# Kernel tuning notes

Hardware: AMD Instinct MI355X
Metric: run time of the kernel (lower is better)

The kernel has to match this reference:

```python
import jax, jax.numpy as jnp
import numpy as np

B, P, Q, D = 16, 4096, 1024, 256


def setup_inputs() -> dict:
    key = jax.random.key(0)
    k1, k2, k3, k4 = jax.random.split(key, 4)
    return {
        "passage_encodes": jax.random.normal(k1, (B, P, D), dtype=jnp.float32),
        "question_encodes": jax.random.normal(k2, (B, Q, D), dtype=jnp.float32),
        "w_attn": jax.random.normal(k3, (2 * D, 1), dtype=jnp.float32) * (1.0 / np.sqrt(2 * D)),
        "b_attn": jnp.zeros((1,), dtype=jnp.float32),
        "w_out": jax.random.normal(k4, (2 * D, 256), dtype=jnp.float32) * (1.0 / np.sqrt(2 * D)),
        "b_out": jnp.zeros((256,), dtype=jnp.float32),
    }


def reference(passage_encodes, question_encodes, w_attn, b_attn, w_out, b_out):
    # similarity matrix [B, P, Q]
    sim = jnp.einsum('bpd,bqd->bpq', passage_encodes, question_encodes)
    # context-to-question attention
    c2q = jax.nn.softmax(sim, axis=-1)                       # [B, P, Q]
    ctx2q = jnp.einsum('bpq,bqd->bpd', c2q, question_encodes)  # [B, P, D]
    # question-to-context attention (softmax over row-max)
    q2c = jax.nn.softmax(jnp.max(sim, axis=-1), axis=-1)     # [B, P]
    q2c_vec = jnp.einsum('bp,bpd->bd', q2c, passage_encodes)  # [B, D]
    tp = jnp.tanh(passage_encodes)
    concat = jnp.concatenate([
        tp * jnp.tanh(ctx2q),
        tp * jnp.tanh(q2c_vec)[:, None, :],  # broadcast instead of repeat
    ], axis=-1)                                              # [B, P, 2D]
    # attention reducer: linear -> softmax over sequence -> weighted sum
    w = jax.nn.softmax(jnp.einsum('bpc,co->bp', concat, w_attn) + b_attn[0], axis=1)
    reduced = jnp.einsum('bp,bpc->bc', w, concat)            # [B, 2D]
    return reduced @ w_out + b_out                            # [B, output_dim]
```

## Files before the change

kernel.cpp:

```cpp
#include <hip/hip_runtime.h>
#include <cmath>

#define BB 16
#define PP 4096
#define QQ 1024
#define DD 256

typedef __attribute__((ext_vector_type(8))) short short8;
typedef __attribute__((ext_vector_type(4))) float floatx4;
typedef __attribute__((ext_vector_type(4))) _Float16 half4;

static __device__ inline ushort bf16_rne(float x) {
  unsigned u = __float_as_uint(x);
  unsigned r = (u + 0x7fffu + ((u >> 16) & 1u)) >> 16;
  return (ushort)r;
}
static __device__ inline float bf16f(ushort h) { return __uint_as_float(((unsigned)h) << 16); }

static __device__ inline float ftanh(float x) {
  float e = __expf(2.0f * x);
  return 1.0f - 2.0f * __builtin_amdgcn_rcpf(e + 1.0f);
}

static __device__ inline void gl16(const void* g, void* l) {
  __builtin_amdgcn_global_load_lds(
      (const __attribute__((address_space(1))) unsigned int*)g,
      (__attribute__((address_space(3))) unsigned int*)l, 16, 0, 0);
}

__global__ __launch_bounds__(256) void kQprep(
    const float* __restrict__ ques, ushort* __restrict__ qb)
{
  const int b = blockIdx.y, qt = blockIdx.x;
  __shared__ float tile[32][260];
  const int tid = threadIdx.x;
  const float* src = ques + ((size_t)b * QQ + qt * 32) * DD;
  for (int i = tid; i < 32 * 64; i += 256) {
    int r = i >> 6, c = (i & 63) << 2;
    *(float4*)&tile[r][c] = *(const float4*)(src + r * DD + c);
  }
  __syncthreads();
  ushort* blob = qb + (size_t)(b * 32 + qt) * 24576;
  {
    int r = tid >> 3;
    int j0 = (tid & 7) * 4;
#pragma unroll
    for (int jj = 0; jj < 4; ++jj) {
      int j = j0 + jj;
      ushort h8[8], l8[8];
#pragma unroll
      for (int e = 0; e < 8; ++e) {
        float x = tile[r][j * 8 + e];
        ushort h = bf16_rne(x);
        h8[e] = h; l8[e] = bf16_rne(x - bf16f(h));
      }
      int g = r * 32 + (j ^ (r & 7));
      *(uint4*)&blob[(size_t)g * 8] = *(uint4*)h8;
      *(uint4*)&blob[8192 + (size_t)g * 8] = *(uint4*)l8;
    }
  }
  {
    int d = tid;
    int s = (d >> 1) & 3;
    ushort h32[32];
#pragma unroll
    for (int r = 0; r < 32; ++r) h32[r] = bf16_rne(tile[r][d]);
#pragma unroll
    for (int k = 0; k < 4; ++k)
      *(uint4*)&blob[16384 + (size_t)d * 32 + (k ^ s) * 8] = *(uint4*)&h32[k * 8];
  }
}

__global__ __launch_bounds__(512, 1) void kA(
    const float* __restrict__ pass, const ushort* __restrict__ qb,
    const float* __restrict__ w_attn,
    _Float16* __restrict__ first_h, _Float16* __restrict__ tp_h,
    float* __restrict__ rowmax, float* __restrict__ logit1)
{
  __shared__ alignas(16) char sm[147456];

  const int b    = blockIdx.y;
  const int p0   = blockIdx.x * 128;
  const int tid  = threadIdx.x;
  const int w    = tid >> 6;
  const int lane = tid & 63;
  const int l15  = lane & 15;
  const int quad = lane >> 4;
  const int swz  = l15 & 7;

  short8 bhi[8], blo[8];
  {
    const float* prow = pass + (((size_t)b * PP + p0 + w * 16 + l15) * DD);
#pragma unroll
    for (int c = 0; c < 8; ++c) {
      const float* p8 = prow + c * 32 + quad * 8;
      float4 x0 = *(const float4*)p8;
      float4 x1 = *(const float4*)(p8 + 4);
      float xs[8] = {x0.x, x0.y, x0.z, x0.w, x1.x, x1.y, x1.z, x1.w};
#pragma unroll
      for (int j = 0; j < 8; ++j) {
        ushort h = bf16_rne(xs[j]);
        ushort lo = bf16_rne(xs[j] - bf16f(h));
        bhi[c][j] = (short)h;
        blo[c][j] = (short)lo;
      }
    }
  }

  int goff[8];
#pragma unroll
  for (int c = 0; c < 8; ++c) goff[c] = (l15 * 32 + ((4 * c + quad) ^ swz)) * 8;
  const int vtoff = l15 * 32 + ((quad ^ ((l15 >> 1) & 3)) * 8);

  const ushort* tb = qb + (size_t)b * 32 * 24576;
  const int dma_l = w * 3072 + lane * 8;
  const int dma_s = w * 6144 + lane * 16;

  floatx4 accO[16];
#pragma unroll
  for (int i = 0; i < 16; ++i) accO[i] = (floatx4){0.f, 0.f, 0.f, 0.f};
  float mx = -INFINITY, ps = 0.f;
  short8 phi = {0, 0, 0, 0, 0, 0, 0, 0}, plo = {0, 0, 0, 0, 0, 0, 0, 0};

  {
    const ushort* gs = tb + dma_l;
    char* ld = sm + dma_s;
#pragma unroll
    for (int i = 0; i < 6; ++i) gl16(gs + i * 512, ld + i * 1024);
  }
  __syncthreads();

  for (int t = 0; t < 32; ++t) {
    const int ic = t % 3, ip = (t + 2) % 3, inx = (t + 1) % 3;
    char* cur = sm + ic * 49152;
    char* prv = sm + ip * 49152;
    if (t < 31) {
      const ushort* gs = tb + (size_t)(t + 1) * 24576 + dma_l;
      char* ld = sm + inx * 49152 + dma_s;
#pragma unroll
      for (int i = 0; i < 6; ++i) gl16(gs + i * 512, ld + i * 1024);
    }

    const ushort* Qhi = (const ushort*)cur;
    const ushort* Qlo = (const ushort*)(cur + 16384);
    floatx4 s0 = (floatx4){0.f, 0.f, 0.f, 0.f};
    floatx4 s1 = (floatx4){0.f, 0.f, 0.f, 0.f};
#pragma unroll
    for (int c = 0; c < 8; ++c) {
      short8 a0h = *(const short8*)&Qhi[goff[c]];
      short8 a0l = *(const short8*)&Qlo[goff[c]];
      short8 a1h = *(const short8*)&Qhi[goff[c] + 4096];
      short8 a1l = *(const short8*)&Qlo[goff[c] + 4096];
      s0 = __builtin_amdgcn_mfma_f32_16x16x32_bf16(a0h, bhi[c], s0, 0, 0, 0);
      s0 = __builtin_amdgcn_mfma_f32_16x16x32_bf16(a0h, blo[c], s0, 0, 0, 0);
      s0 = __builtin_amdgcn_mfma_f32_16x16x32_bf16(a0l, bhi[c], s0, 0, 0, 0);
      s1 = __builtin_amdgcn_mfma_f32_16x16x32_bf16(a1h, bhi[c], s1, 0, 0, 0);
      s1 = __builtin_amdgcn_mfma_f32_16x16x32_bf16(a1h, blo[c], s1, 0, 0, 0);
      s1 = __builtin_amdgcn_mfma_f32_16x16x32_bf16(a1l, bhi[c], s1, 0, 0, 0);
    }

    if (t > 0) {
      const ushort* TQ = (const ushort*)(prv + 32768);
#pragma unroll
      for (int nt = 0; nt < 16; ++nt) {
        short8 vhi = *(const short8*)&TQ[nt * 512 + vtoff];
        accO[nt] = __builtin_amdgcn_mfma_f32_16x16x32_bf16(phi, vhi, accO[nt], 0, 0, 0);
        accO[nt] = __builtin_amdgcn_mfma_f32_16x16x32_bf16(plo, vhi, accO[nt], 0, 0, 0);
      }
    }

    float pv[8];
#pragma unroll
    for (int r = 0; r < 4; ++r) {
      float s = s0[r];
      mx = fmaxf(mx, s);
      pv[r] = __expf(s - 60.f);
      ps += pv[r];
    }
#pragma unroll
    for (int r = 0; r < 4; ++r) {
      float s = s1[r];
      mx = fmaxf(mx, s);
      pv[4 + r] = __expf(s - 60.f);
      ps += pv[4 + r];
    }

    unsigned* pwv = (unsigned*)prv + w * 512;
#pragma unroll
    for (int mt = 0; mt < 2; ++mt) {
      unsigned pk[4];
#pragma unroll
      for (int r = 0; r < 4; ++r) {
        float x = pv[mt * 4 + r];
        ushort h = bf16_rne(x);
        ushort lo = bf16_rne(x - bf16f(h));
        pk[r] = (unsigned)h | ((unsigned)lo << 16);
      }
      int g = l15 * 8 + ((mt * 4 + quad) ^ swz);
      *(uint4*)&pwv[g * 4] = *(uint4*)pk;
    }
    uint4 u0 = *(const uint4*)&pwv[(l15 * 8 + ((2 * quad) ^ swz)) * 4];
    uint4 u1 = *(const uint4*)&pwv[(l15 * 8 + ((2 * quad + 1) ^ swz)) * 4];
    unsigned ua[8] = {u0.x, u0.y, u0.z, u0.w, u1.x, u1.y, u1.z, u1.w};
#pragma unroll
    for (int j = 0; j < 8; ++j) {
      phi[j] = (short)(ua[j] & 0xffffu);
      plo[j] = (short)(ua[j] >> 16);
    }
    __syncthreads();
  }

  {
    const ushort* TQ = (const ushort*)(sm + 49152 + 32768);
#pragma unroll
    for (int nt = 0; nt < 16; ++nt) {
      short8 vhi = *(const short8*)&TQ[nt * 512 + vtoff];
      accO[nt] = __builtin_amdgcn_mfma_f32_16x16x32_bf16(phi, vhi, accO[nt], 0, 0, 0);
      accO[nt] = __builtin_amdgcn_mfma_f32_16x16x32_bf16(plo, vhi, accO[nt], 0, 0, 0);
    }
  }

  ps += __shfl_xor(ps, 16);
  ps += __shfl_xor(ps, 32);
  mx = fmaxf(mx, __shfl_xor(mx, 16));
  mx = fmaxf(mx, __shfl_xor(mx, 32));

  __syncthreads();
  float* Of = (float*)(sm + w * 16640);
#pragma unroll
  for (int nt = 0; nt < 16; ++nt)
#pragma unroll
    for (int r = 0; r < 4; ++r)
      Of[(quad * 4 + r) * 260 + nt * 16 + l15] = accO[nt][r];
  const float4 w1 = *(const float4*)(w_attn + lane * 4);
  const size_t rowoff = (size_t)b * PP + p0 + w * 16;
#pragma unroll
  for (int j = 0; j < 16; ++j) {
    float4 o = *(const float4*)&Of[j * 260 + lane * 4];
    float linv = 1.f / __shfl(ps, j);
    float4 pv4 = *(const float4*)(pass + (rowoff + j) * DD + lane * 4);
    float tpx = ftanh(pv4.x), tpy = ftanh(pv4.y), tpz = ftanh(pv4.z), tpw = ftanh(pv4.w);
    float4 f;
    f.x = tpx * ftanh(o.x * linv);
    f.y = tpy * ftanh(o.y * linv);
    f.z = tpz * ftanh(o.z * linv);
    f.w = tpw * ftanh(o.w * linv);
    half4 fh = {(_Float16)f.x, (_Float16)f.y, (_Float16)f.z, (_Float16)f.w};
    half4 th = {(_Float16)tpx, (_Float16)tpy, (_Float16)tpz, (_Float16)tpw};
    *(half4*)(first_h + (rowoff + j) * DD + lane * 4) = fh;
    *(half4*)(tp_h + (rowoff + j) * DD + lane * 4) = th;
    float part = f.x * w1.x + f.y * w1.y + f.z * w1.z + f.w * w1.w;
    part += __shfl_xor(part, 1);  part += __shfl_xor(part, 2);
    part += __shfl_xor(part, 4);  part += __shfl_xor(part, 8);
    part += __shfl_xor(part, 16); part += __shfl_xor(part, 32);
    if (lane == 0) logit1[rowoff + j] = part;
  }
  if (lane < 16) rowmax[rowoff + lane] = mx;
}

__global__ __launch_bounds__(256) void kB2(
    const float* __restrict__ pass, const float* __restrict__ rowmax,
    float* __restrict__ numpart, float* __restrict__ denpart)
{
  const int b = blockIdx.y, chunk = blockIdx.x;
  const int tid = threadIdx.x, r = tid >> 6, ln = tid & 63;
  __shared__ float sacc[4][64][4];
  __shared__ float sden[4][64];
  const float* rm = rowmax + (size_t)b * PP + chunk * 128;
  const float* pb = pass + ((size_t)b * PP + chunk * 128) * DD;
  float4 acc = make_float4(0.f, 0.f, 0.f, 0.f);
  float den = 0.f;
  for (int p = r; p < 128; p += 4) {
    float wgt = __expf(rm[p] - 60.f);
    float4 v = *(const float4*)(pb + (size_t)p * DD + ln * 4);
    acc.x += wgt * v.x; acc.y += wgt * v.y;
    acc.z += wgt * v.z; acc.w += wgt * v.w;
    den += wgt;
  }
  *(float4*)&sacc[r][ln][0] = acc;
  sden[r][ln] = den;
  __syncthreads();
  if (r == 0) {
    float4 s;
    s.x = sacc[0][ln][0] + sacc[1][ln][0] + sacc[2][ln][0] + sacc[3][ln][0];
    s.y = sacc[0][ln][1] + sacc[1][ln][1] + sacc[2][ln][1] + sacc[3][ln][1];
    s.z = sacc[0][ln][2] + sacc[1][ln][2] + sacc[2][ln][2] + sacc[3][ln][2];
    s.w = sacc[0][ln][3] + sacc[1][ln][3] + sacc[2][ln][3] + sacc[3][ln][3];
    *(float4*)(numpart + (size_t)(chunk * 16 + b) * DD + ln * 4) = s;
    if (ln == 0)
      denpart[chunk * 16 + b] = sden[0][0] + sden[1][0] + sden[2][0] + sden[3][0];
  }
}

__global__ void kB3(const float* __restrict__ numpart, const float* __restrict__ denpart,
                    const float* __restrict__ w_attn,
                    float* __restrict__ tq, float* __restrict__ w2tq)
{
  const int b = blockIdx.x, d = threadIdx.x;
  float den = 0.f, num = 0.f;
#pragma unroll
  for (int c = 0; c < 32; ++c) {
    den += denpart[c * 16 + b];
    num += numpart[(size_t)(c * 16 + b) * DD + d];
  }
  float t = ftanh(num / den);
  tq[b * DD + d] = t;
  w2tq[b * DD + d] = w_attn[DD + d] * t;
}

__global__ __launch_bounds__(256) void kC(
    const _Float16* __restrict__ tp_h, const float* __restrict__ logit1,
    const float* __restrict__ w2tq, float* __restrict__ el)
{
  const int b = blockIdx.y, chunk = blockIdx.x;
  const int wave = threadIdx.x >> 6, lane = threadIdx.x & 63;
  const float4 wv = *(const float4*)(w2tq + b * DD + (lane << 2));
  const int pbase = chunk * 128 + wave * 32;
  for (int j = 0; j < 32; ++j) {
    int p = pbase + j;
    half4 tv = *(const half4*)(tp_h + ((size_t)b * PP + p) * DD + (lane << 2));
    float part = (float)tv.x * wv.x + (float)tv.y * wv.y +
                 (float)tv.z * wv.z + (float)tv.w * wv.w;
    part += __shfl_xor(part, 1);  part += __shfl_xor(part, 2);
    part += __shfl_xor(part, 4);  part += __shfl_xor(part, 8);
    part += __shfl_xor(part, 16); part += __shfl_xor(part, 32);
    if (lane == 0)
      el[(size_t)b * PP + p] = __expf(logit1[(size_t)b * PP + p] + part);
  }
}

__global__ __launch_bounds__(256) void kE(
    const _Float16* __restrict__ tp_h, const _Float16* __restrict__ first_h,
    const float* __restrict__ el,
    float* __restrict__ r1part, float* __restrict__ r2part, float* __restrict__ den2part)
{
  const int b = blockIdx.y, chunk = blockIdx.x;
  const int tid = threadIdx.x, r = tid >> 6, ln = tid & 63;
  __shared__ float s1[4][64][4];
  __shared__ float s2[4][64][4];
  __shared__ float sd[4][64];
  const float* ev = el + (size_t)b * PP + chunk * 128;
  const size_t base = ((size_t)b * PP + chunk * 128) * DD;
  float a1[4] = {0.f, 0.f, 0.f, 0.f}, a2[4] = {0.f, 0.f, 0.f, 0.f};
  float den = 0.f;
  for (int p = r; p < 128; p += 4) {
    float wgt = ev[p];
    half4 f = *(const half4*)(first_h + base + (size_t)p * DD + ln * 4);
    half4 t = *(const half4*)(tp_h + base + (size_t)p * DD + ln * 4);
    a1[0] += wgt * (float)f.x; a1[1] += wgt * (float)f.y;
    a1[2] += wgt * (float)f.z; a1[3] += wgt * (float)f.w;
    a2[0] += wgt * (float)t.x; a2[1] += wgt * (float)t.y;
    a2[2] += wgt * (float)t.z; a2[3] += wgt * (float)t.w;
    den += wgt;
  }
  *(float4*)&s1[r][ln][0] = *(float4*)a1;
  *(float4*)&s2[r][ln][0] = *(float4*)a2;
  sd[r][ln] = den;
  __syncthreads();
  if (r == 0) {
    float o1[4], o2[4];
#pragma unroll
    for (int i = 0; i < 4; ++i) {
      o1[i] = s1[0][ln][i] + s1[1][ln][i] + s1[2][ln][i] + s1[3][ln][i];
      o2[i] = s2[0][ln][i] + s2[1][ln][i] + s2[2][ln][i] + s2[3][ln][i];
    }
    *(float4*)(r1part + (size_t)(chunk * 16 + b) * DD + ln * 4) = *(float4*)o1;
    *(float4*)(r2part + (size_t)(chunk * 16 + b) * DD + ln * 4) = *(float4*)o2;
    if (ln == 0)
      den2part[chunk * 16 + b] = sd[0][0] + sd[1][0] + sd[2][0] + sd[3][0];
  }
}

__global__ __launch_bounds__(256) void kF(
    const float* __restrict__ r1part, const float* __restrict__ r2part,
    const float* __restrict__ den2part, const float* __restrict__ tq,
    const float* __restrict__ w_out, const float* __restrict__ b_out,
    float* __restrict__ out)
{
  const int b = blockIdx.x, o = threadIdx.x;
  __shared__ float R1[256], R2[256];
  float den = 0.f, red1 = 0.f, red2 = 0.f;
#pragma unroll
  for (int c = 0; c < 32; ++c) {
    den += den2part[c * 16 + b];
    red1 += r1part[(size_t)(c * 16 + b) * DD + o];
    red2 += r2part[(size_t)(c * 16 + b) * DD + o];
  }
  float inv = 1.f / den;
  R1[o] = red1 * inv;
  R2[o] = red2 * inv * tq[b * DD + o];
  __syncthreads();
  float acc = b_out[o];
  for (int k = 0; k < DD; ++k)
    acc += R1[k] * w_out[k * 256 + o];
  for (int k = 0; k < DD; ++k)
    acc += R2[k] * w_out[(DD + k) * 256 + o];
  out[b * 256 + o] = acc;
}

extern "C" void kernel_launch(void* const* d_in, const int* in_sizes, int n_in,
                              void* d_out, int out_size, void* d_ws, size_t ws_size,
                              hipStream_t stream) {
  const float* pass   = (const float*)d_in[0];
  const float* ques   = (const float*)d_in[1];
  const float* w_attn = (const float*)d_in[2];
  const float* w_out  = (const float*)d_in[4];
  const float* b_out  = (const float*)d_in[5];
  float* out = (float*)d_out;

  float* ws       = (float*)d_ws;
  float* rowmax   = ws;
  float* logit1   = rowmax   + (size_t)BB * PP;
  float* el       = logit1   + (size_t)BB * PP;
  float* numpart  = el       + (size_t)BB * PP;
  float* denpart  = numpart  + (size_t)32 * BB * DD;
  float* r1part   = denpart  + 32 * BB;
  float* r2part   = r1part   + (size_t)32 * BB * DD;
  float* den2part = r2part   + (size_t)32 * BB * DD;
  float* tq       = den2part + 32 * BB;
  float* w2tq     = tq       + BB * DD;
  ushort* qbb     = (ushort*)(w2tq + BB * DD);
  _Float16* first_h = (_Float16*)(qbb + (size_t)BB * 32 * 24576);
  _Float16* tp_h    = first_h + (size_t)BB * PP * DD;

  kQprep<<<dim3(QQ / 32, BB), 256, 0, stream>>>(ques, qbb);
  kA    <<<dim3(PP / 128, BB), 512, 0, stream>>>(pass, qbb, w_attn,
                                                 first_h, tp_h, rowmax, logit1);
  kB2   <<<dim3(32, BB), 256, 0, stream>>>(pass, rowmax, numpart, denpart);
  kB3   <<<BB, 256, 0, stream>>>(numpart, denpart, w_attn, tq, w2tq);
  kC    <<<dim3(32, BB), 256, 0, stream>>>(tp_h, logit1, w2tq, el);
  kE    <<<dim3(32, BB), 256, 0, stream>>>(tp_h, first_h, el, r1part, r2part, den2part);
  kF    <<<BB, 256, 0, stream>>>(r1part, r2part, den2part, tq, w_out, b_out, out);
}
```

Baseline: 352.3 us.

## Re-tile attention kernel warps over Q halves and D groups with LDS P exchange

Each warp now computes scores for two 16-row passage tiles against one half of each Q chunk, so Q fragments are reused across two tiles. P is written to a shared LDS buffer and the PV product is split so each warp accumulates a 64x64 output block. Partial sums and maxes are combined through LDS. The triple buffer becomes a double buffer, shared memory shrinks, launch bounds request two blocks per CU, and setprio hints are added. The cost is an extra barrier per iteration, and the PV step now runs in the same iteration as the scores instead of being overlapped one step behind.

After: 381.1 us. 8.2% more time.

```diff
diff --git a/kernel.cpp b/kernel.cpp
--- a/kernel.cpp
+++ b/kernel.cpp
@@ -9,6 +9,7 @@
 typedef __attribute__((ext_vector_type(8))) short short8;
 typedef __attribute__((ext_vector_type(4))) float floatx4;
 typedef __attribute__((ext_vector_type(4))) _Float16 half4;
+typedef __attribute__((ext_vector_type(4))) unsigned short ushort4v;
 
 static __device__ inline ushort bf16_rne(float x) {
   unsigned u = __float_as_uint(x);
@@ -71,13 +72,13 @@
   }
 }
 
-__global__ __launch_bounds__(512, 1) void kA(
+__global__ __launch_bounds__(512, 2) void kA(
     const float* __restrict__ pass, const ushort* __restrict__ qb,
     const float* __restrict__ w_attn,
     _Float16* __restrict__ first_h, _Float16* __restrict__ tp_h,
     float* __restrict__ rowmax, float* __restrict__ logit1)
 {
-  __shared__ alignas(16) char sm[147456];
+  __shared__ alignas(16) char sm[135168];
 
   const int b    = blockIdx.y;
   const int p0   = blockIdx.x * 128;
@@ -88,9 +89,15 @@
   const int quad = lane >> 4;
   const int swz  = l15 & 7;
 
-  short8 bhi[8], blo[8];
-  {
-    const float* prow = pass + (((size_t)b * PP + p0 + w * 16 + l15) * DD);
+  const int qt1  = w >> 2;
+  const int pt1  = (w & 3) * 2;
+  const int dgrp = w >> 1;
+  const int phs  = (w & 1) * 4;
+
+  short8 bhi[2][8], blo[2][8];
+#pragma unroll
+  for (int pt = 0; pt < 2; ++pt) {
+    const float* prow = pass + (((size_t)b * PP + p0 + (pt1 + pt) * 16 + l15) * DD);
 #pragma unroll
     for (int c = 0; c < 8; ++c) {
       const float* p8 = prow + c * 32 + quad * 8;
@@ -99,28 +106,32 @@
       float xs[8] = {x0.x, x0.y, x0.z, x0.w, x1.x, x1.y, x1.z, x1.w};
 #pragma unroll
       for (int j = 0; j < 8; ++j) {
-        ushort h = bf16_rne(xs[j]);
+        ushort h  = bf16_rne(xs[j]);
         ushort lo = bf16_rne(xs[j] - bf16f(h));
-        bhi[c][j] = (short)h;
-        blo[c][j] = (short)lo;
+        bhi[pt][c][j] = (short)h;
+        blo[pt][c][j] = (short)lo;
       }
     }
   }
 
-  int goff[8];
-#pragma unroll
-  for (int c = 0; c < 8; ++c) goff[c] = (l15 * 32 + ((4 * c + quad) ^ swz)) * 8;
+  const int gb    = (qt1 * 16 + l15) * 256;
   const int vtoff = l15 * 32 + ((quad ^ ((l15 >> 1) & 3)) * 8);
+
+  ushort* PbufH = (ushort*)(sm + 98304);
+  ushort* PbufL = (ushort*)(sm + 106496);
+  const int pgd  = qt1 * 2 + (quad >> 1);
+  const int psub = (quad & 1) * 4;
 
   const ushort* tb = qb + (size_t)b * 32 * 24576;
   const int dma_l = w * 3072 + lane * 8;
   const int dma_s = w * 6144 + lane * 16;
 
-  floatx4 accO[16];
-#pragma unroll
-  for (int i = 0; i < 16; ++i) accO[i] = (floatx4){0.f, 0.f, 0.f, 0.f};
-  float mx = -INFINITY, ps = 0.f;
-  short8 phi = {0, 0, 0, 0, 0, 0, 0, 0}, plo = {0, 0, 0, 0, 0, 0, 0, 0};
+  floatx4 accO[4][4];
+#pragma unroll
+  for (int i = 0; i < 4; ++i)
+#pragma unroll
+    for (int k = 0; k < 4; ++k) accO[i][k] = (floatx4){0.f, 0.f, 0.f, 0.f};
+  float ps0 = 0.f, ps1 = 0.f, mx0 = -INFINITY, mx1 = -INFINITY;
 
   {
     const ushort* gs = tb + dma_l;
@@ -131,12 +142,10 @@
   __syncthreads();
 
   for (int t = 0; t < 32; ++t) {
-    const int ic = t % 3, ip = (t + 2) % 3, inx = (t + 1) % 3;
-    char* cur = sm + ic * 49152;
-    char* prv = sm + ip * 49152;
+    const char* cur = sm + (t & 1) * 49152;
     if (t < 31) {
       const ushort* gs = tb + (size_t)(t + 1) * 24576 + dma_l;
-      char* ld = sm + inx * 49152 + dma_s;
+      char* ld = sm + ((t + 1) & 1) * 49152 + dma_s;
 #pragma unroll
       for (int i = 0; i < 6; ++i) gl16(gs + i * 512, ld + i * 1024);
     }
@@ -145,99 +154,114 @@
     const ushort* Qlo = (const ushort*)(cur + 16384);
     floatx4 s0 = (floatx4){0.f, 0.f, 0.f, 0.f};
     floatx4 s1 = (floatx4){0.f, 0.f, 0.f, 0.f};
+    __builtin_amdgcn_s_setprio(1);
 #pragma unroll
     for (int c = 0; c < 8; ++c) {
-      short8 a0h = *(const short8*)&Qhi[goff[c]];
-      short8 a0l = *(const short8*)&Qlo[goff[c]];
-      short8 a1h = *(const short8*)&Qhi[goff[c] + 4096];
-      short8 a1l = *(const short8*)&Qlo[goff[c] + 4096];
-      s0 = __builtin_amdgcn_mfma_f32_16x16x32_bf16(a0h, bhi[c], s0, 0, 0, 0);
-      s0 = __builtin_amdgcn_mfma_f32_16x16x32_bf16(a0h, blo[c], s0, 0, 0, 0);
-      s0 = __builtin_amdgcn_mfma_f32_16x16x32_bf16(a0l, bhi[c], s0, 0, 0, 0);
-      s1 = __builtin_amdgcn_mfma_f32_16x16x32_bf16(a1h, bhi[c], s1, 0, 0, 0);
-      s1 = __builtin_amdgcn_mfma_f32_16x16x32_bf16(a1h, blo[c], s1, 0, 0, 0);
-      s1 = __builtin_amdgcn_mfma_f32_16x16x32_bf16(a1l, bhi[c], s1, 0, 0, 0);
-    }
-
-    if (t > 0) {
-      const ushort* TQ = (const ushort*)(prv + 32768);
-#pragma unroll
-      for (int nt = 0; nt < 16; ++nt) {
-        short8 vhi = *(const short8*)&TQ[nt * 512 + vtoff];
-        accO[nt] = __builtin_amdgcn_mfma_f32_16x16x32_bf16(phi, vhi, accO[nt], 0, 0, 0);
-        accO[nt] = __builtin_amdgcn_mfma_f32_16x16x32_bf16(plo, vhi, accO[nt], 0, 0, 0);
+      const int go = gb + (((4 * c + quad) ^ swz) << 3);
+      short8 ah = *(const short8*)&Qhi[go];
+      short8 al = *(const short8*)&Qlo[go];
+      s0 = __builtin_amdgcn_mfma_f32_16x16x32_bf16(ah, bhi[0][c], s0, 0, 0, 0);
+      s0 = __builtin_amdgcn_mfma_f32_16x16x32_bf16(ah, blo[0][c], s0, 0, 0, 0);
+      s0 = __builtin_amdgcn_mfma_f32_16x16x32_bf16(al, bhi[0][c], s0, 0, 0, 0);
+      s1 = __builtin_amdgcn_mfma_f32_16x16x32_bf16(ah, bhi[1][c], s1, 0, 0, 0);
+      s1 = __builtin_amdgcn_mfma_f32_16x16x32_bf16(ah, blo[1][c], s1, 0, 0, 0);
+      s1 = __builtin_amdgcn_mfma_f32_16x16x32_bf16(al, bhi[1][c], s1, 0, 0, 0);
+    }
+    __builtin_amdgcn_s_setprio(0);
+
+    {
+      ushort4v ph, pl;
+#pragma unroll
+      for (int r = 0; r < 4; ++r) {
+        float s = s0[r];
+        mx0 = fmaxf(mx0, s);
+        float x = __expf(s - 60.f);
+        ps0 += x;
+        ushort h = bf16_rne(x);
+        ph[r] = h;
+        pl[r] = bf16_rne(x - bf16f(h));
       }
-    }
-
-    float pv[8];
-#pragma unroll
-    for (int r = 0; r < 4; ++r) {
-      float s = s0[r];
-      mx = fmaxf(mx, s);
-      pv[r] = __expf(s - 60.f);
-      ps += pv[r];
-    }
-#pragma unroll
-    for (int r = 0; r < 4; ++r) {
-      float s = s1[r];
-      mx = fmaxf(mx, s);
-      pv[4 + r] = __expf(s - 60.f);
-      ps += pv[4 + r];
-    }
-
-    unsigned* pwv = (unsigned*)prv + w * 512;
-#pragma unroll
-    for (int mt = 0; mt < 2; ++mt) {
-      unsigned pk[4];
+      const int wi = ((pt1 * 16 + l15) * 4 + (pgd ^ (l15 & 3))) * 8 + psub;
+      *(ushort4v*)&PbufH[wi] = ph;
+      *(ushort4v*)&PbufL[wi] = pl;
+    }
+    {
+      ushort4v ph, pl;
 #pragma unroll
       for (int r = 0; r < 4; ++r) {
-        float x = pv[mt * 4 + r];
+        float s = s1[r];
+        mx1 = fmaxf(mx1, s);
+        float x = __expf(s - 60.f);
+        ps1 += x;
         ushort h = bf16_rne(x);
-        ushort lo = bf16_rne(x - bf16f(h));
-        pk[r] = (unsigned)h | ((unsigned)lo << 16);
+        ph[r] = h;
+        pl[r] = bf16_rne(x - bf16f(h));
       }
-      int g = l15 * 8 + ((mt * 4 + quad) ^ swz);
-      *(uint4*)&pwv[g * 4] = *(uint4*)pk;
-    }
-    uint4 u0 = *(const uint4*)&pwv[(l15 * 8 + ((2 * quad) ^ swz)) * 4];
-    uint4 u1 = *(const uint4*)&pwv[(l15 * 8 + ((2 * quad + 1) ^ swz)) * 4];
-    unsigned ua[8] = {u0.x, u0.y, u0.z, u0.w, u1.x, u1.y, u1.z, u1.w};
-#pragma unroll
-    for (int j = 0; j < 8; ++j) {
-      phi[j] = (short)(ua[j] & 0xffffu);
-      plo[j] = (short)(ua[j] >> 16);
-    }
+      const int wi = (((pt1 + 1) * 16 + l15) * 4 + (pgd ^ (l15 & 3))) * 8 + psub;
+      *(ushort4v*)&PbufH[wi] = ph;
+      *(ushort4v*)&PbufL[wi] = pl;
+    }
+
+    asm volatile("s_waitcnt lgkmcnt(0)" ::: "memory");
+    __builtin_amdgcn_s_barrier();
+    __builtin_amdgcn_sched_barrier(0);
+
+    const ushort* TQ = (const ushort*)(cur + 32768);
+    short8 vhi[4];
+#pragma unroll
+    for (int k = 0; k < 4; ++k)
+      vhi[k] = *(const short8*)&TQ[(dgrp * 4 + k) * 512 + vtoff];
+    __builtin_amdgcn_s_setprio(1);
+#pragma unroll
+    for (int pt = 0; pt < 4; ++pt) {
+      const int ri = (((phs + pt) * 16 + l15) * 4 + (quad ^ (l15 & 3))) * 8;
+      short8 phh = *(const short8*)&PbufH[ri];
+      short8 pll = *(const short8*)&PbufL[ri];
+#pragma unroll
+      for (int k = 0; k < 4; ++k) {
+        accO[pt][k] = __builtin_amdgcn_mfma_f32_16x16x32_bf16(phh, vhi[k], accO[pt][k], 0, 0, 0);
+        accO[pt][k] = __builtin_amdgcn_mfma_f32_16x16x32_bf16(pll, vhi[k], accO[pt][k], 0, 0, 0);
+      }
+    }
+    __builtin_amdgcn_s_setprio(0);
     __syncthreads();
   }
 
-  {
-    const ushort* TQ = (const ushort*)(sm + 49152 + 32768);
-#pragma unroll
-    for (int nt = 0; nt < 16; ++nt) {
-      short8 vhi = *(const short8*)&TQ[nt * 512 + vtoff];
-      accO[nt] = __builtin_amdgcn_mfma_f32_16x16x32_bf16(phi, vhi, accO[nt], 0, 0, 0);
-      accO[nt] = __builtin_amdgcn_mfma_f32_16x16x32_bf16(plo, vhi, accO[nt], 0, 0, 0);
-    }
-  }
-
-  ps += __shfl_xor(ps, 16);
-  ps += __shfl_xor(ps, 32);
-  mx = fmaxf(mx, __shfl_xor(mx, 16));
-  mx = fmaxf(mx, __shfl_xor(mx, 32));
-
-  __syncthreads();
-  float* Of = (float*)(sm + w * 16640);
-#pragma unroll
-  for (int nt = 0; nt < 16; ++nt)
-#pragma unroll
-    for (int r = 0; r < 4; ++r)
-      Of[(quad * 4 + r) * 260 + nt * 16 + l15] = accO[nt][r];
+  ps0 += __shfl_xor(ps0, 16); ps0 += __shfl_xor(ps0, 32);
+  ps1 += __shfl_xor(ps1, 16); ps1 += __shfl_xor(ps1, 32);
+  mx0 = fmaxf(mx0, __shfl_xor(mx0, 16)); mx0 = fmaxf(mx0, __shfl_xor(mx0, 32));
+  mx1 = fmaxf(mx1, __shfl_xor(mx1, 16)); mx1 = fmaxf(mx1, __shfl_xor(mx1, 32));
+
+  float* psb = (float*)(sm + 133120);
+  float* mxb = (float*)(sm + 134144);
+  if (lane < 16) {
+    psb[(qt1 * 8 + pt1) * 16 + l15]     = ps0;
+    psb[(qt1 * 8 + pt1 + 1) * 16 + l15] = ps1;
+    mxb[(qt1 * 8 + pt1) * 16 + l15]     = mx0;
+    mxb[(qt1 * 8 + pt1 + 1) * 16 + l15] = mx1;
+  }
+  __syncthreads();
+  const float pstot = psb[w * 16 + l15] + psb[128 + w * 16 + l15];
+  const float mxtot = fmaxf(mxb[w * 16 + l15], mxb[128 + w * 16 + l15]);
+  const size_t rowoff = (size_t)b * PP + p0 + w * 16;
+  if (lane < 16) rowmax[rowoff + lane] = mxtot;
+
+  float* Of = (float*)sm;
+#pragma unroll
+  for (int pt = 0; pt < 4; ++pt)
+#pragma unroll
+    for (int k = 0; k < 4; ++k)
+#pragma unroll
+      for (int r = 0; r < 4; ++r)
+        Of[((w & 1) * 64 + pt * 16 + quad * 4 + r) * 260 + dgrp * 64 + k * 16 + l15] =
+            accO[pt][k][r];
+  __syncthreads();
+
   const float4 w1 = *(const float4*)(w_attn + lane * 4);
-  const size_t rowoff = (size_t)b * PP + p0 + w * 16;
 #pragma unroll
   for (int j = 0; j < 16; ++j) {
-    float4 o = *(const float4*)&Of[j * 260 + lane * 4];
-    float linv = 1.f / __shfl(ps, j);
+    float4 o = *(const float4*)&Of[(w * 16 + j) * 260 + lane * 4];
+    float linv = 1.f / __shfl(pstot, j);
     float4 pv4 = *(const float4*)(pass + (rowoff + j) * DD + lane * 4);
     float tpx = ftanh(pv4.x), tpy = ftanh(pv4.y), tpz = ftanh(pv4.z), tpw = ftanh(pv4.w);
     float4 f;
@@ -255,7 +279,6 @@
     part += __shfl_xor(part, 16); part += __shfl_xor(part, 32);
     if (lane == 0) logit1[rowoff + j] = part;
   }
-  if (lane < 16) rowmax[rowoff + lane] = mx;
 }
 
 __global__ __launch_bounds__(256) void kB2(
```

## Fuse q2c reduction into attention kernel and logit exp into reducer

Applied to the files above, without the earlier changes.

The q2c weighted sum over passage rows moves into kA's epilogue. It reuses the passage row already loaded there and the row max held in registers, which removes kB2 and its second full read of the passage tensor. kC is folded into kE, which now computes the tp·w2tq dot product and the exp inline, so the separate el buffer and one extra read of tp_h go away. The hi part of the bf16 split is now made by truncation instead of round-to-nearest, so the lo residual compensates and precision stays the same. In exchange kA gets extra LDS reduction work and an extra barrier at its tail.

Result: faster. 328.3 us (-6.8%).

```diff
diff --git a/kernel.cpp b/kernel.cpp
--- a/kernel.cpp
+++ b/kernel.cpp
@@ -75,7 +75,8 @@
     const float* __restrict__ pass, const ushort* __restrict__ qb,
     const float* __restrict__ w_attn,
     _Float16* __restrict__ first_h, _Float16* __restrict__ tp_h,
-    float* __restrict__ rowmax, float* __restrict__ logit1)
+    float* __restrict__ logit1,
+    float* __restrict__ numpart, float* __restrict__ denpart)
 {
   __shared__ alignas(16) char sm[147456];
 
@@ -192,9 +193,10 @@
 #pragma unroll
       for (int r = 0; r < 4; ++r) {
         float x = pv[mt * 4 + r];
-        ushort h = bf16_rne(x);
-        ushort lo = bf16_rne(x - bf16f(h));
-        pk[r] = (unsigned)h | ((unsigned)lo << 16);
+        unsigned u = __float_as_uint(x);
+        unsigned hb = u & 0xffff0000u;
+        ushort lo = bf16_rne(x - __uint_as_float(hb));
+        pk[r] = (hb >> 16) | ((unsigned)lo << 16);
       }
       int g = l15 * 8 + ((mt * 4 + quad) ^ swz);
       *(uint4*)&pwv[g * 4] = *(uint4*)pk;
@@ -234,11 +236,17 @@
       Of[(quad * 4 + r) * 260 + nt * 16 + l15] = accO[nt][r];
   const float4 w1 = *(const float4*)(w_attn + lane * 4);
   const size_t rowoff = (size_t)b * PP + p0 + w * 16;
+  float4 qacc = make_float4(0.f, 0.f, 0.f, 0.f);
+  float dacc = 0.f;
 #pragma unroll
   for (int j = 0; j < 16; ++j) {
     float4 o = *(const float4*)&Of[j * 260 + lane * 4];
     float linv = 1.f / __shfl(ps, j);
     float4 pv4 = *(const float4*)(pass + (rowoff + j) * DD + lane * 4);
+    float wj = __expf(__shfl(mx, j) - 60.f);
+    qacc.x += wj * pv4.x; qacc.y += wj * pv4.y;
+    qacc.z += wj * pv4.z; qacc.w += wj * pv4.w;
+    dacc += wj;
     float tpx = ftanh(pv4.x), tpy = ftanh(pv4.y), tpz = ftanh(pv4.z), tpw = ftanh(pv4.w);
     float4 f;
     f.x = tpx * ftanh(o.x * linv);
@@ -255,40 +263,23 @@
     part += __shfl_xor(part, 16); part += __shfl_xor(part, 32);
     if (lane == 0) logit1[rowoff + j] = part;
   }
-  if (lane < 16) rowmax[rowoff + lane] = mx;
-}
-
-__global__ __launch_bounds__(256) void kB2(
-    const float* __restrict__ pass, const float* __restrict__ rowmax,
-    float* __restrict__ numpart, float* __restrict__ denpart)
-{
-  const int b = blockIdx.y, chunk = blockIdx.x;
-  const int tid = threadIdx.x, r = tid >> 6, ln = tid & 63;
-  __shared__ float sacc[4][64][4];
-  __shared__ float sden[4][64];
-  const float* rm = rowmax + (size_t)b * PP + chunk * 128;
-  const float* pb = pass + ((size_t)b * PP + chunk * 128) * DD;
-  float4 acc = make_float4(0.f, 0.f, 0.f, 0.f);
-  float den = 0.f;
-  for (int p = r; p < 128; p += 4) {
-    float wgt = __expf(rm[p] - 60.f);
-    float4 v = *(const float4*)(pb + (size_t)p * DD + ln * 4);
-    acc.x += wgt * v.x; acc.y += wgt * v.y;
-    acc.z += wgt * v.z; acc.w += wgt * v.w;
-    den += wgt;
-  }
-  *(float4*)&sacc[r][ln][0] = acc;
-  sden[r][ln] = den;
-  __syncthreads();
-  if (r == 0) {
-    float4 s;
-    s.x = sacc[0][ln][0] + sacc[1][ln][0] + sacc[2][ln][0] + sacc[3][ln][0];
-    s.y = sacc[0][ln][1] + sacc[1][ln][1] + sacc[2][ln][1] + sacc[3][ln][1];
-    s.z = sacc[0][ln][2] + sacc[1][ln][2] + sacc[2][ln][2] + sacc[3][ln][2];
-    s.w = sacc[0][ln][3] + sacc[1][ln][3] + sacc[2][ln][3] + sacc[3][ln][3];
-    *(float4*)(numpart + (size_t)(chunk * 16 + b) * DD + ln * 4) = s;
-    if (ln == 0)
-      denpart[chunk * 16 + b] = sden[0][0] + sden[1][0] + sden[2][0] + sden[3][0];
+
+  float* redw = (float*)(sm + w * 16640);
+  *(float4*)&redw[lane * 4] = qacc;
+  if (lane == 0) redw[256] = dacc;
+  __syncthreads();
+  if (w == 0) {
+    float4 s = make_float4(0.f, 0.f, 0.f, 0.f);
+    float dsum = 0.f;
+#pragma unroll
+    for (int wv = 0; wv < 8; ++wv) {
+      const float* rp = (const float*)(sm + wv * 16640);
+      float4 v = *(const float4*)&rp[lane * 4];
+      s.x += v.x; s.y += v.y; s.z += v.z; s.w += v.w;
+      dsum += rp[256];
+    }
+    *(float4*)(numpart + (size_t)(blockIdx.x * 16 + b) * DD + lane * 4) = s;
+    if (lane == 0) denpart[blockIdx.x * 16 + b] = dsum;
   }
 }
 
@@ -308,30 +299,9 @@
   w2tq[b * DD + d] = w_attn[DD + d] * t;
 }
 
-__global__ __launch_bounds__(256) void kC(
-    const _Float16* __restrict__ tp_h, const float* __restrict__ logit1,
-    const float* __restrict__ w2tq, float* __restrict__ el)
-{
-  const int b = blockIdx.y, chunk = blockIdx.x;
-  const int wave = threadIdx.x >> 6, lane = threadIdx.x & 63;
-  const float4 wv = *(const float4*)(w2tq + b * DD + (lane << 2));
-  const int pbase = chunk * 128 + wave * 32;
-  for (int j = 0; j < 32; ++j) {
-    int p = pbase + j;
-    half4 tv = *(const half4*)(tp_h + ((size_t)b * PP + p) * DD + (lane << 2));
-    float part = (float)tv.x * wv.x + (float)tv.y * wv.y +
-                 (float)tv.z * wv.z + (float)tv.w * wv.w;
-    part += __shfl_xor(part, 1);  part += __shfl_xor(part, 2);
-    part += __shfl_xor(part, 4);  part += __shfl_xor(part, 8);
-    part += __shfl_xor(part, 16); part += __shfl_xor(part, 32);
-    if (lane == 0)
-      el[(size_t)b * PP + p] = __expf(logit1[(size_t)b * PP + p] + part);
-  }
-}
-
 __global__ __launch_bounds__(256) void kE(
     const _Float16* __restrict__ tp_h, const _Float16* __restrict__ first_h,
-    const float* __restrict__ el,
+    const float* __restrict__ logit1, const float* __restrict__ w2tq,
     float* __restrict__ r1part, float* __restrict__ r2part, float* __restrict__ den2part)
 {
   const int b = blockIdx.y, chunk = blockIdx.x;
@@ -339,14 +309,20 @@
   __shared__ float s1[4][64][4];
   __shared__ float s2[4][64][4];
   __shared__ float sd[4][64];
-  const float* ev = el + (size_t)b * PP + chunk * 128;
+  const float4 wv = *(const float4*)(w2tq + b * DD + (ln << 2));
+  const float* lg = logit1 + (size_t)b * PP + chunk * 128;
   const size_t base = ((size_t)b * PP + chunk * 128) * DD;
   float a1[4] = {0.f, 0.f, 0.f, 0.f}, a2[4] = {0.f, 0.f, 0.f, 0.f};
   float den = 0.f;
   for (int p = r; p < 128; p += 4) {
-    float wgt = ev[p];
     half4 f = *(const half4*)(first_h + base + (size_t)p * DD + ln * 4);
     half4 t = *(const half4*)(tp_h + base + (size_t)p * DD + ln * 4);
+    float part = (float)t.x * wv.x + (float)t.y * wv.y +
+                 (float)t.z * wv.z + (float)t.w * wv.w;
+    part += __shfl_xor(part, 1);  part += __shfl_xor(part, 2);
+    part += __shfl_xor(part, 4);  part += __shfl_xor(part, 8);
+    part += __shfl_xor(part, 16); part += __shfl_xor(part, 32);
+    float wgt = __expf(lg[p] + part);
     a1[0] += wgt * (float)f.x; a1[1] += wgt * (float)f.y;
     a1[2] += wgt * (float)f.z; a1[3] += wgt * (float)f.w;
     a2[0] += wgt * (float)t.x; a2[1] += wgt * (float)t.y;
@@ -425,10 +401,10 @@
 
   kQprep<<<dim3(QQ / 32, BB), 256, 0, stream>>>(ques, qbb);
   kA    <<<dim3(PP / 128, BB), 512, 0, stream>>>(pass, qbb, w_attn,
-                                                 first_h, tp_h, rowmax, logit1);
-  kB2   <<<dim3(32, BB), 256, 0, stream>>>(pass, rowmax, numpart, denpart);
+                                                 first_h, tp_h, logit1,
+                                                 numpart, denpart);
   kB3   <<<BB, 256, 0, stream>>>(numpart, denpart, w_attn, tq, w2tq);
-  kC    <<<dim3(32, BB), 256, 0, stream>>>(tp_h, logit1, w2tq, el);
-  kE    <<<dim3(32, BB), 256, 0, stream>>>(tp_h, first_h, el, r1part, r2part, den2part);
+  kE    <<<dim3(32, BB), 256, 0, stream>>>(tp_h, first_h, logit1, w2tq,
+                                           r1part, r2part, den2part);
   kF    <<<BB, 256, 0, stream>>>(r1part, r2part, den2part, tq, w_out, b_out, out);
 }
```
